# Kernel optimization log

Hardware: AMD Instinct MI355X
Metric: run time of the kernel (lower is better)

## Reference

```python
import jax, jax.numpy as jnp
import numpy as np

TEMPERATURE = 22.627417  # ~sqrt(512)


def setup_inputs() -> dict:
    key = jax.random.key(0)
    ks = jax.random.split(key, 7)
    B, NP, NQ, D = 4, 256, 256, 512
    return {
        "q": jax.random.normal(ks[0], (B, NP, D), jnp.float32),
        "k": jax.random.normal(ks[1], (B, NP, D), jnp.float32),
        "v": jax.random.normal(ks[2], (B, NP, D), jnp.float32),
        "query": jax.random.normal(ks[3], (B, NQ, D), jnp.float32),
        "query_q": jax.random.normal(ks[4], (B, NQ, D), jnp.float32),
        "query_k": jax.random.normal(ks[5], (B, NP, D), jnp.float32),
        "query_v": jax.random.normal(ks[6], (B, NQ, D), jnp.float32),
    }


def reference(q, k, v, query, query_q, query_k, query_v):
    # Self-attention block over prototypes: [B, NP, NP]
    scores = jnp.einsum("bpd,bqd->bpq", q, k) / TEMPERATURE
    log_attn = jax.nn.log_softmax(scores, axis=2)
    attn = jax.nn.softmax(scores, axis=2)
    # NOTE: torch.bmm(attn, v) in the original is dead code (overwritten), so it is skipped.

    # Query-gated attention: [B, NQ, NP]
    q_scores = jnp.einsum("bnd,bpd->bnp", query_q, query_k) / TEMPERATURE
    query_attn = jax.nn.softmax(q_scores, axis=2)

    # Gated broadcast combine: [B, NQ, NP, D]
    # query_attn * v_rep + query_attn * query_v == query_attn * (v + query_v)
    gate = query_attn[:, :, :, None]            # [B, NQ, NP, 1]
    combined = v[:, None, :, :] + query_v[:, :, None, :]  # [B, NQ, NP, D]
    output = gate * combined
    return (output, attn, log_attn)
```

## Files before the change

kernel.cpp:

```cpp
#include <hip/hip_runtime.h>
#include <math.h>

#define BB   4
#define NP   256
#define NQ   256
#define DD   512
#define DD4  (DD / 4)

#define NSTORE       1792
#define TOTAL_CHUNKS 131072

typedef float f32x4 __attribute__((ext_vector_type(4)));

static constexpr float kScale = 1.0f / 22.627417f;

__global__ __launch_bounds__(256) void gate_kernel(
    const float* __restrict__ qq,
    const float* __restrict__ qk,
    float* __restrict__ gws)
{
    const int b  = blockIdx.y;
    const int n0 = blockIdx.x * 4;
    const int t  = threadIdx.x;

    const f32x4* krow = (const f32x4*)(qk + ((size_t)b * NP + t) * DD);
    const float* qb   = qq + ((size_t)b * NQ + n0) * DD;

    float acc[4] = {0.f, 0.f, 0.f, 0.f};
    #pragma unroll 8
    for (int d4 = 0; d4 < DD4; ++d4) {
        const f32x4 kv = krow[d4];
        #pragma unroll
        for (int r = 0; r < 4; ++r) {
            const float* qr = qb + r * DD + d4 * 4;
            acc[r] += qr[0] * kv.x + qr[1] * kv.y + qr[2] * kv.z + qr[3] * kv.w;
        }
    }

    __shared__ __align__(16) float ss[4][256];
    #pragma unroll
    for (int r = 0; r < 4; ++r) ss[r][t] = acc[r] * kScale;
    __syncthreads();

    const int r = t >> 6;
    const int g = t & 63;
    const f32x4 sv = ((const f32x4*)ss[r])[g];

    float m = fmaxf(fmaxf(sv.x, sv.y), fmaxf(sv.z, sv.w));
    #pragma unroll
    for (int off = 32; off >= 1; off >>= 1) m = fmaxf(m, __shfl_xor(m, off, 64));

    f32x4 ev;
    ev.x = expf(sv.x - m); ev.y = expf(sv.y - m);
    ev.z = expf(sv.z - m); ev.w = expf(sv.w - m);
    float s = (ev.x + ev.y) + (ev.z + ev.w);
    #pragma unroll
    for (int off = 32; off >= 1; off >>= 1) s += __shfl_xor(s, off, 64);

    ((f32x4*)(gws + ((size_t)b * NQ + n0 + r) * NP))[g] = ev * (1.0f / s);
}

__global__ __launch_bounds__(256) void store_kernel(
    const float* __restrict__ q,
    const float* __restrict__ k,
    const f32x4* __restrict__ v4,
    const f32x4* __restrict__ qv4,
    const float* __restrict__ gws,
    f32x4* __restrict__ out4,
    float* __restrict__ attn_out,
    float* __restrict__ logattn_out)
{
    const int t = threadIdx.x;

    if (blockIdx.x < (unsigned)NSTORE) {
        const int h  = t >> 7;
        const int d4 = t & (DD4 - 1);

        for (int c = blockIdx.x; c < TOTAL_CHUNKS; c += NSTORE) {
            const int b = c >> 15;
            const int n = (c >> 7) & 255;
            const int p = (2 * c + h) & 255;

            int gidx = (((b << 8) + n) << 8) + p;
            gidx = __builtin_amdgcn_readfirstlane(gidx);
            const float gpn = gws[gidx];

            const f32x4 vv  = v4[(((size_t)(b << 8) + p) << 7) + d4];
            const f32x4 qvv = qv4[(((size_t)(b << 8) + n) << 7) + d4];
            __builtin_nontemporal_store((vv + qvv) * gpn,
                                        out4 + ((size_t)c << 8) + t);
        }
    } else {
        const int idx = blockIdx.x - NSTORE;
        const int b   = idx >> 6;
        const int p0  = (idx & 63) * 4;

        const f32x4* krow = (const f32x4*)(k + ((size_t)b * NP + t) * DD);
        const float* qb   = q + ((size_t)b * NP + p0) * DD;

        float acc[4] = {0.f, 0.f, 0.f, 0.f};
        #pragma unroll 8
        for (int d4 = 0; d4 < DD4; ++d4) {
            const f32x4 kv = krow[d4];
            #pragma unroll
            for (int r = 0; r < 4; ++r) {
                const float* qr = qb + r * DD + d4 * 4;
                acc[r] += qr[0] * kv.x + qr[1] * kv.y + qr[2] * kv.z + qr[3] * kv.w;
            }
        }

        __shared__ __align__(16) float ss[4][256];
        #pragma unroll
        for (int r = 0; r < 4; ++r) ss[r][t] = acc[r] * kScale;
        __syncthreads();

        const int r = t >> 6;
        const int g = t & 63;
        const f32x4 sv = ((const f32x4*)ss[r])[g];

        float m = fmaxf(fmaxf(sv.x, sv.y), fmaxf(sv.z, sv.w));
        #pragma unroll
        for (int off = 32; off >= 1; off >>= 1)
            m = fmaxf(m, __shfl_xor(m, off, 64));

        f32x4 ev;
        ev.x = expf(sv.x - m); ev.y = expf(sv.y - m);
        ev.z = expf(sv.z - m); ev.w = expf(sv.w - m);
        float s = (ev.x + ev.y) + (ev.z + ev.w);
        #pragma unroll
        for (int off = 32; off >= 1; off >>= 1) s += __shfl_xor(s, off, 64);

        const float inv = 1.0f / s;
        const float lse = logf(s);

        const size_t base = ((size_t)b * NP + (p0 + r)) * 256;
        ((f32x4*)(attn_out + base))[g] = ev * inv;
        f32x4 lg;
        lg.x = (sv.x - m) - lse; lg.y = (sv.y - m) - lse;
        lg.z = (sv.z - m) - lse; lg.w = (sv.w - m) - lse;
        ((f32x4*)(logattn_out + base))[g] = lg;
    }
}

extern "C" void kernel_launch(void* const* d_in, const int* in_sizes, int n_in,
                              void* d_out, int out_size, void* d_ws, size_t ws_size,
                              hipStream_t stream) {
    const float* q  = (const float*)d_in[0];
    const float* k  = (const float*)d_in[1];
    const float* v  = (const float*)d_in[2];
    const float* qq = (const float*)d_in[4];
    const float* qk = (const float*)d_in[5];
    const float* qv = (const float*)d_in[6];

    float* out = (float*)d_out;
    const size_t out_elems = (size_t)BB * NQ * NP * DD;
    float* attn_out    = out + out_elems;
    float* logattn_out = attn_out + (size_t)BB * NP * 256;

    float* gws = (float*)d_ws;

    gate_kernel<<<dim3(NQ / 4, BB), 256, 0, stream>>>(qq, qk, gws);

    store_kernel<<<NSTORE + 256, 256, 0, stream>>>(
        q, k, (const f32x4*)v, (const f32x4*)qv, gws,
        (f32x4*)out, attn_out, logattn_out);
}
```

Measured before the change: 134.7 us.

## Tile broadcast store into 8x16 (n,p) blocks with register reuse of v and query_v

Replaces the grid-stride per-row store loop with one block per 8 query x 16 prototype tile. Each block loads 8 v rows and 8 query_v rows into registers and the gate tile into shared memory, then writes 64 output rows, cutting repeated loads of v and query_v. The self-attention blocks now come first in the grid. Stores are no longer nontemporal, which may change cache behaviour for the large streaming output, and register pressure rises.

```diff
diff --git a/kernel.cpp b/kernel.cpp
--- a/kernel.cpp
+++ b/kernel.cpp
@@ -6,9 +6,6 @@
 #define NQ   256
 #define DD   512
 #define DD4  (DD / 4)
-
-#define NSTORE       1792
-#define TOTAL_CHUNKS 131072
 
 typedef float f32x4 __attribute__((ext_vector_type(4)));
 
@@ -72,26 +69,41 @@
 {
     const int t = threadIdx.x;
 
-    if (blockIdx.x < (unsigned)NSTORE) {
-        const int h  = t >> 7;
-        const int d4 = t & (DD4 - 1);
+    if (blockIdx.x >= 256u) {
+        const int idx = blockIdx.x - 256;
+        const int b   = idx >> 9;
+        const int r   = idx & 511;
+        const int n0  = (r >> 4) << 3;
+        const int p0  = (r & 15) << 4;
+        const int d4  = t & (DD4 - 1);
+        const int h   = t >> 7;
 
-        for (int c = blockIdx.x; c < TOTAL_CHUNKS; c += NSTORE) {
-            const int b = c >> 15;
-            const int n = (c >> 7) & 255;
-            const int p = (2 * c + h) & 255;
+        __shared__ float gl[8][16];
+        if (t < 128)
+            gl[t >> 4][t & 15] =
+                gws[((size_t)b * NQ + n0 + (t >> 4)) * NP + p0 + (t & 15)];
+        __syncthreads();
 
-            int gidx = (((b << 8) + n) << 8) + p;
-            gidx = __builtin_amdgcn_readfirstlane(gidx);
-            const float gpn = gws[gidx];
+        const f32x4* vb  = v4  + (((size_t)b * NP + p0) << 7) + d4;
+        const f32x4* qvb = qv4 + (((size_t)b * NQ + n0) << 7) + d4;
+        f32x4 vv[8], qvv[8];
+        #pragma unroll
+        for (int i = 0; i < 8; ++i) vv[i]  = vb[(size_t)(2 * i + h) << 7];
+        #pragma unroll
+        for (int j = 0; j < 8; ++j) qvv[j] = qvb[(size_t)j << 7];
 
-            const f32x4 vv  = v4[(((size_t)(b << 8) + p) << 7) + d4];
-            const f32x4 qvv = qv4[(((size_t)(b << 8) + n) << 7) + d4];
-            __builtin_nontemporal_store((vv + qvv) * gpn,
-                                        out4 + ((size_t)c << 8) + t);
+        f32x4* ob = out4 + ((((size_t)b * NQ + n0) * NP + p0) << 7) + d4;
+        #pragma unroll
+        for (int j = 0; j < 8; ++j) {
+            f32x4* obn = ob + (((size_t)j * NP) << 7);
+            #pragma unroll
+            for (int i = 0; i < 8; ++i) {
+                const int pc = 2 * i + h;
+                obn[(size_t)pc << 7] = (vv[i] + qvv[j]) * gl[j][pc];
+            }
         }
     } else {
-        const int idx = blockIdx.x - NSTORE;
+        const int idx = blockIdx.x;
         const int b   = idx >> 6;
         const int p0  = (idx & 63) * 4;
 
@@ -161,7 +173,7 @@
 
     gate_kernel<<<dim3(NQ / 4, BB), 256, 0, stream>>>(qq, qk, gws);
 
-    store_kernel<<<NSTORE + 256, 256, 0, stream>>>(
+    store_kernel<<<256 + 2048, 256, 0, stream>>>(
         q, k, (const f32x4*)v, (const f32x4*)qv, gws,
         (f32x4*)out, attn_out, logattn_out);
 }
```

New measurement: 144.0 us. 1.07x slower.
